# Kernel tuning notes

Measured on AMD Instinct MI355X. Metric: run time of the kernel, lower is better.

The kernel has to match this reference:

```python
import jax, jax.numpy as jnp
import numpy as np

N, N1, N2, K = 65536, 16384, 8192, 16
INDIM, HID, OUT = 64, 32, 128


def _knn_np(pos, q, k, chunk=1024):
    # brute-force chunked KNN (indices into pos) for setup only
    out = []
    for s in range(0, q.shape[0], chunk):
        d = ((q[s:s + chunk, None, :] - pos[None, :, :]) ** 2).sum(-1)
        out.append(np.argpartition(d, k, axis=1)[:, :k])
    return np.concatenate(out, 0)


def setup_inputs() -> dict:
    key = jax.random.key(0)
    ks = jax.random.split(key, 12)
    x = jax.random.normal(ks[0], (N, INDIM), jnp.float32)
    pos = jax.random.uniform(ks[1], (N, 3), jnp.float32)

    pos_np = np.asarray(pos)
    rng = np.random.default_rng(0)
    idx1 = np.sort(rng.choice(N, N1, replace=False))            # RandomSampler(ratio1)
    nn1 = _knn_np(pos_np, pos_np[idx1], K)                      # [N1, K] into full cloud
    src1, dst1 = nn1.reshape(-1), np.repeat(np.arange(N1), K)
    pos1 = pos_np[idx1]
    idx2 = np.sort(rng.choice(N1, N2, replace=False))           # RandomSampler(ratio2)
    nn2 = _knn_np(pos1, pos1[idx2], K)                          # [N2, K] into level-1 cloud
    src2, dst2 = nn2.reshape(-1), np.repeat(np.arange(N2), K)

    def lin(k, i, o):
        return jax.random.normal(k, (i, o), jnp.float32) / float(np.sqrt(i))

    return dict(
        x=x, pos=pos,
        W_down=lin(ks[2], INDIM, HID), b_down=jnp.zeros((HID,), jnp.float32),
        W_pp1=lin(ks[3], 10, 32), b_pp1=jnp.zeros((32,), jnp.float32),
        W_att1=lin(ks[4], 64, 64), b_att1=jnp.zeros((64,), jnp.float32),
        W_g1=lin(ks[5], 64, 64), b_g1=jnp.zeros((64,), jnp.float32),
        W_pp2=lin(ks[6], 10, 64), b_pp2=jnp.zeros((64,), jnp.float32),
        W_att2=lin(ks[7], 128, 128), b_att2=jnp.zeros((128,), jnp.float32),
        W_g2=lin(ks[8], 128, 128), b_g2=jnp.zeros((128,), jnp.float32),
        W_up=lin(ks[9], 128, OUT), b_up=jnp.zeros((OUT,), jnp.float32),
        W_sc=lin(ks[10], INDIM, OUT), b_sc=jnp.zeros((OUT,), jnp.float32),
        idx1=jnp.asarray(idx1, jnp.int32), idx2=jnp.asarray(idx2, jnp.int32),
        src1=jnp.asarray(src1, jnp.int32), dst1=jnp.asarray(dst1, jnp.int32),
        src2=jnp.asarray(src2, jnp.int32), dst2=jnp.asarray(dst2, jnp.int32),
    )


def _mlp(h, W, b):
    return jax.nn.relu(h @ W + b)


def _randla_conv(x, pos_all, pos_q, src, dst, Wpp, bpp, Watt, batt, Wg, bg, n_out):
    # RandlaKernel.message + add-aggregate + update (bipartite: targets = sampled points)
    pos_i, pos_j = pos_q[dst], pos_all[src]                     # [E,3]
    vij = pos_i - pos_j
    dij = jnp.sqrt((vij * vij).sum(-1, keepdims=True))          # [E,1]
    rel = jnp.concatenate([pos_i, pos_j, vij, dij], axis=1)     # [E,10]
    rij = _mlp(rel, Wpp, bpp)                                   # point_pos_nn
    fij = jnp.concatenate([x[src], rij], axis=1)                # [E, c+d]
    s = jax.nn.softmax(_mlp(fij, Watt, batt), axis=-1)          # softmax over feature dim (as in source)
    agg = jax.ops.segment_sum(s * fij, dst, num_segments=n_out) # aggr='add'
    return _mlp(agg, Wg, bg)                                    # global_nn


def reference(x, pos, W_down, b_down, W_pp1, b_pp1, W_att1, b_att1, W_g1, b_g1,
              W_pp2, b_pp2, W_att2, b_att2, W_g2, b_g2, W_up, b_up, W_sc, b_sc,
              idx1, idx2, src1, dst1, src2, dst2):
    h = _mlp(x, W_down, b_down)                                 # features_downsample (indim -> outdim//4)
    pos1 = pos[idx1]
    h = _randla_conv(h, pos, pos1, src1, dst1, W_pp1, b_pp1, W_att1, b_att1, W_g1, b_g1, N1)
    pos2 = pos1[idx2]
    h = _randla_conv(h, pos1, pos2, src2, dst2, W_pp2, b_pp2, W_att2, b_att2, W_g2, b_g2, N2)
    h = _mlp(h, W_up, b_up)                                     # features_upsample
    sc = _mlp(x[idx1][idx2], W_sc, b_sc)                        # shortcut resized, idx = idx1[idx2]
    return jax.nn.relu(h + sc)
```

## Files before the change

kernel.cpp:

```cpp
#include <hip/hip_runtime.h>

#define N_FULL 65536
#define NN1    16384
#define NN2    8192

typedef __attribute__((ext_vector_type(8))) short bf16x8;
typedef __attribute__((ext_vector_type(4))) float f32x4;
typedef unsigned short ushortT;

#define MFMA16(acc, a, b) acc = __builtin_amdgcn_mfma_f32_16x16x32_bf16(a, b, acc, 0, 0, 0)

#if __has_builtin(__builtin_amdgcn_cvt_pk_bf16_f32)
typedef __attribute__((ext_vector_type(2))) __bf16 bf16x2t;
static __device__ __forceinline__ unsigned pack2(float a, float b) {
    union { bf16x2t v; unsigned u; } c;
    c.v = __builtin_amdgcn_cvt_pk_bf16_f32(a, b);
    return c.u;
}
static __device__ __forceinline__ ushortT f2bf(float f) {
    union { bf16x2t v; ushortT s[2]; } c;
    c.v = __builtin_amdgcn_cvt_pk_bf16_f32(f, 0.f);
    return c.s[0];
}
#else
static __device__ __forceinline__ ushortT f2bf(float f) {
    union { float f; unsigned u; } v; v.f = f;
    unsigned r = v.u + 0x7FFFu + ((v.u >> 16) & 1u);
    return (ushortT)(r >> 16);
}
static __device__ __forceinline__ unsigned pack2(float a, float b) {
    return (unsigned)f2bf(a) | ((unsigned)f2bf(b) << 16);
}
#endif

static __device__ __forceinline__ float bfu2f(ushortT h) {
    union { unsigned u; float f; } v; v.u = (unsigned)h << 16; return v.f;
}

#define WS_WAT1  2304
#define WS_WGT1  6912
#define WS_WAT2  11520
#define WS_WGT2  28928
#define WS_WUPT  46336
#define WS_WSCT  63744
#define WS_H0    73728
#define WS_H1    (WS_H0 + 65536u*32u)

#define SMAX_SHIFT 24.0f

static __device__ __forceinline__ void tpose(
    const float* __restrict__ src, ushortT* __restrict__ dst,
    int K, int N, int STR, int gid, int gs)
{
    for (int i = gid; i < K * N; i += gs) {
        const int n = i / K, k = i - n * K;
        dst[n * STR + k] = f2bf(src[(size_t)k * N + n]);
    }
}

__global__ __launch_bounds__(256) void k_down(
    const float* __restrict__ x, const float* __restrict__ Wd,
    const float* __restrict__ bd,
    const float* __restrict__ Wa1, const float* __restrict__ Wg1,
    const float* __restrict__ Wa2, const float* __restrict__ Wg2,
    const float* __restrict__ Wup, const float* __restrict__ Wsc,
    ushortT* __restrict__ wsw, ushortT* __restrict__ h0w)
{
    const int t = threadIdx.x;
    if (blockIdx.x >= 512) {
        const int gid = (blockIdx.x - 512) * 256 + t, gs = 68 * 256;
        tpose(Wa1, wsw + WS_WAT1, 64, 64, 72, gid, gs);
        tpose(Wg1, wsw + WS_WGT1, 64, 64, 72, gid, gs);
        tpose(Wa2, wsw + WS_WAT2, 128, 128, 136, gid, gs);
        tpose(Wg2, wsw + WS_WGT2, 128, 128, 136, gid, gs);
        tpose(Wup, wsw + WS_WUPT, 128, 128, 136, gid, gs);
        tpose(Wsc, wsw + WS_WSCT, 64, 128, 72, gid, gs);
        return;
    }

    __shared__ __align__(16) ushortT Al[128 * 72];
    __shared__ __align__(16) ushortT Bl[32 * 72];
    const int rowBase = blockIdx.x * 128;

    {
        const int r = t >> 1, c0 = (t & 1) * 32;
        unsigned* dst = (unsigned*)Al + r * 36 + (c0 >> 1);
        const float* src = &x[(size_t)(rowBase + r) * 64 + c0];
#pragma unroll
        for (int j = 0; j < 32; j += 4) {
            const float4 v = *reinterpret_cast<const float4*>(src + j);
            dst[(j >> 1) + 0] = pack2(v.x, v.y);
            dst[(j >> 1) + 1] = pack2(v.z, v.w);
        }
        const int n = t >> 3, kc = (t & 7) * 8;
        float v[8];
#pragma unroll
        for (int j = 0; j < 8; ++j) v[j] = Wd[(size_t)(kc + j) * 32 + n];
        uint4 p;
        p.x = pack2(v[0], v[1]); p.y = pack2(v[2], v[3]);
        p.z = pack2(v[4], v[5]); p.w = pack2(v[6], v[7]);
        *(uint4*)((unsigned*)Bl + n * 36 + (kc >> 1)) = p;
    }
    __syncthreads();

    const int lane = t & 63, w = t >> 6, quad = lane >> 4, c16 = lane & 15;
    f32x4 acc[2][2];
#pragma unroll
    for (int mt = 0; mt < 2; ++mt)
#pragma unroll
        for (int nt = 0; nt < 2; ++nt)
#pragma unroll
            for (int r = 0; r < 4; ++r) acc[mt][nt][r] = 0.f;
#pragma unroll
    for (int ks = 0; ks < 2; ++ks) {
        bf16x8 a[2], b[2];
#pragma unroll
        for (int mt = 0; mt < 2; ++mt)
            a[mt] = *(const bf16x8*)&Al[(w * 32 + mt * 16 + c16) * 72 + ks * 32 + quad * 8];
#pragma unroll
        for (int nt = 0; nt < 2; ++nt)
            b[nt] = *(const bf16x8*)&Bl[(nt * 16 + c16) * 72 + ks * 32 + quad * 8];
#pragma unroll
        for (int mt = 0; mt < 2; ++mt)
#pragma unroll
            for (int nt = 0; nt < 2; ++nt) MFMA16(acc[mt][nt], a[mt], b[nt]);
    }
#pragma unroll
    for (int nt = 0; nt < 2; ++nt) {
        const int col = nt * 16 + c16;
        const float bias = bd[col];
#pragma unroll
        for (int mt = 0; mt < 2; ++mt)
#pragma unroll
            for (int r = 0; r < 4; ++r) {
                const int row = rowBase + w * 32 + mt * 16 + quad * 4 + r;
                h0w[(size_t)row * 32 + col] = f2bf(fmaxf(acc[mt][nt][r] + bias, 0.f));
            }
    }
}

__global__ __launch_bounds__(512) void k_conv1(
    const ushortT* __restrict__ h0w, const float* __restrict__ pos,
    const int* __restrict__ idx1, const int* __restrict__ src1,
    const float* __restrict__ Wpp, const float* __restrict__ bpp,
    const ushortT* __restrict__ wsw, const float* __restrict__ batt,
    const float* __restrict__ bg, ushortT* __restrict__ h1w)
{
    __shared__ __align__(16) ushortT Fl[128 * 72];
    __shared__ __align__(16) ushortT A2ls[16 * 72];
    __shared__ float Pl[352];
    const int t = threadIdx.x;
    const int d0 = blockIdx.x * 8;

    for (int i = t; i < 352; i += 512) Pl[i] = (i < 320) ? Wpp[i] : bpp[i - 320];
    for (int i = t; i < 288; i += 512) ((unsigned*)A2ls)[288 + i] = 0;

    {
        const int e = t >> 2, q = t & 3;
        const int g = e >> 4;
        const int s = src1[(d0 + g) * 16 + (e & 15)];
        ((uint4*)((unsigned*)Fl + e * 36))[q] =
            ((const uint4*)((const unsigned*)h0w + (size_t)s * 16))[q];

        const int pin = idx1[d0 + g];
        const float pix = pos[pin * 3 + 0], piy = pos[pin * 3 + 1], piz = pos[pin * 3 + 2];
        const float pjx = pos[s * 3 + 0],  pjy = pos[s * 3 + 1],  pjz = pos[s * 3 + 2];
        const float vx = pix - pjx, vy = piy - pjy, vz = piz - pjz;
        const float dij = sqrtf(vx * vx + vy * vy + vz * vz);
        const float rel[10] = {pix, piy, piz, pjx, pjy, pjz, vx, vy, vz, dij};
        __syncthreads();
        const int c0 = q * 8;
#pragma unroll
        for (int c = 0; c < 8; c += 2) {
            float a0 = Pl[320 + c0 + c], a1 = Pl[320 + c0 + c + 1];
#pragma unroll
            for (int i = 0; i < 10; ++i) {
                a0 += rel[i] * Pl[i * 32 + c0 + c];
                a1 += rel[i] * Pl[i * 32 + c0 + c + 1];
            }
            ((unsigned*)Fl)[(e * 72 + 32 + c0 + c) >> 1] = pack2(fmaxf(a0, 0.f), fmaxf(a1, 0.f));
        }
    }
    __syncthreads();

    const int lane = t & 63, w = t >> 6, quad = lane >> 4, c16 = lane & 15;
    const ushortT* WB = wsw + WS_WAT1;
    f32x4 acc[4];
#pragma unroll
    for (int nt = 0; nt < 4; ++nt)
#pragma unroll
        for (int r = 0; r < 4; ++r) acc[nt][r] = 0.f;
#pragma unroll
    for (int ks = 0; ks < 2; ++ks) {
        const bf16x8 a = *(const bf16x8*)&Fl[(w * 16 + c16) * 72 + ks * 32 + quad * 8];
#pragma unroll
        for (int nt = 0; nt < 4; ++nt) {
            const bf16x8 b = *(const bf16x8*)&WB[(nt * 16 + c16) * 72 + ks * 32 + quad * 8];
            MFMA16(acc[nt], a, b);
        }
    }
    float bcol[4];
#pragma unroll
    for (int nt = 0; nt < 4; ++nt) bcol[nt] = batt[nt * 16 + c16];

    float rs[4];
#pragma unroll
    for (int r = 0; r < 4; ++r) {
        float sm = 0.f;
#pragma unroll
        for (int nt = 0; nt < 4; ++nt) {
            const float a = fmaxf(acc[nt][r] + bcol[nt], 0.f);
            acc[nt][r] = __expf(a - SMAX_SHIFT);
            sm += acc[nt][r];
        }
        sm += __shfl_xor(sm, 1);
        sm += __shfl_xor(sm, 2);
        sm += __shfl_xor(sm, 4);
        sm += __shfl_xor(sm, 8);
        rs[r] = 1.f / sm;
    }
#pragma unroll
    for (int nt = 0; nt < 4; ++nt) {
        float v = 0.f;
#pragma unroll
        for (int r = 0; r < 4; ++r) {
            const float fv = bfu2f(Fl[(w * 16 + quad * 4 + r) * 72 + nt * 16 + c16]);
            v += acc[nt][r] * rs[r] * fv;
        }
        v += __shfl_xor(v, 16);
        v += __shfl_xor(v, 32);
        if (lane < 16)
            A2ls[w * 72 + nt * 16 + c16] = f2bf(v);
    }
    __syncthreads();

    if (w < 4) {
        const ushortT* GB = wsw + WS_WGT1;
        f32x4 acc2 = {0.f, 0.f, 0.f, 0.f};
#pragma unroll
        for (int ks = 0; ks < 2; ++ks) {
            const bf16x8 a = *(const bf16x8*)&A2ls[c16 * 72 + ks * 32 + quad * 8];
            const bf16x8 b = *(const bf16x8*)&GB[(w * 16 + c16) * 72 + ks * 32 + quad * 8];
            MFMA16(acc2, a, b);
        }
        const int col = w * 16 + c16;
        const float bias = bg[col];
        if (quad < 2) {
#pragma unroll
            for (int r = 0; r < 4; ++r) {
                const int row = quad * 4 + r;
                h1w[(size_t)(d0 + row) * 64 + col] = f2bf(fmaxf(acc2[r] + bias, 0.f));
            }
        }
    }
}

__global__ __launch_bounds__(512) void k_conv2f(
    const ushortT* __restrict__ h1w, const float* __restrict__ pos,
    const float* __restrict__ x,
    const int* __restrict__ idx1, const int* __restrict__ idx2,
    const int* __restrict__ src2,
    const float* __restrict__ Wpp, const float* __restrict__ bpp,
    const ushortT* __restrict__ wsw, const float* __restrict__ batt,
    const float* __restrict__ bg, const float* __restrict__ bup,
    const float* __restrict__ bsc, float* __restrict__ out)
{
    __shared__ __align__(16) ushortT Fl[128 * 136];
    __shared__ __align__(16) ushortT AGG[16 * 136];
    __shared__ __align__(16) ushortT H2[16 * 136];
    __shared__ float Pl[704];
    const int t = threadIdx.x;
    const int d0 = blockIdx.x * 8;

    for (int i = t; i < 704; i += 512) Pl[i] = (i < 640) ? Wpp[i] : bpp[i - 640];
    for (int i = t; i < 544; i += 512) ((unsigned*)AGG)[544 + i] = 0;

    {
        const int e = t >> 2, q = t & 3;
        const int g = e >> 4;
        const int s = src2[(d0 + g) * 16 + (e & 15)];
        {
            const uint4* srcp = (const uint4*)((const unsigned*)h1w + (size_t)s * 32);
            uint4* dstp = (uint4*)((unsigned*)Fl + e * 68);
            dstp[q * 2 + 0] = srcp[q * 2 + 0];
            dstp[q * 2 + 1] = srcp[q * 2 + 1];
        }
        const int pin = idx1[idx2[d0 + g]];
        const int sn = idx1[s];
        const float pix = pos[pin * 3 + 0], piy = pos[pin * 3 + 1], piz = pos[pin * 3 + 2];
        const float pjx = pos[sn * 3 + 0],  pjy = pos[sn * 3 + 1],  pjz = pos[sn * 3 + 2];
        const float vx = pix - pjx, vy = piy - pjy, vz = piz - pjz;
        const float dij = sqrtf(vx * vx + vy * vy + vz * vz);
        const float rel[10] = {pix, piy, piz, pjx, pjy, pjz, vx, vy, vz, dij};
        __syncthreads();
        const int c0 = q * 16;
#pragma unroll
        for (int c = 0; c < 16; c += 2) {
            float a0 = Pl[640 + c0 + c], a1 = Pl[640 + c0 + c + 1];
#pragma unroll
            for (int i = 0; i < 10; ++i) {
                a0 += rel[i] * Pl[i * 64 + c0 + c];
                a1 += rel[i] * Pl[i * 64 + c0 + c + 1];
            }
            ((unsigned*)Fl)[(e * 136 + 64 + c0 + c) >> 1] = pack2(fmaxf(a0, 0.f), fmaxf(a1, 0.f));
        }
    }
    __syncthreads();

    const int lane = t & 63, w = t >> 6, quad = lane >> 4, c16 = lane & 15;
    const ushortT* WB = wsw + WS_WAT2;
    f32x4 acc[8];
#pragma unroll
    for (int nt = 0; nt < 8; ++nt)
#pragma unroll
        for (int r = 0; r < 4; ++r) acc[nt][r] = 0.f;
#pragma unroll
    for (int ks = 0; ks < 4; ++ks) {
        const bf16x8 a = *(const bf16x8*)&Fl[(w * 16 + c16) * 136 + ks * 32 + quad * 8];
#pragma unroll
        for (int nt = 0; nt < 8; ++nt) {
            const bf16x8 b = *(const bf16x8*)&WB[(nt * 16 + c16) * 136 + ks * 32 + quad * 8];
            MFMA16(acc[nt], a, b);
        }
    }
    float bcol[8];
#pragma unroll
    for (int nt = 0; nt < 8; ++nt) bcol[nt] = batt[nt * 16 + c16];

    float rs[4];
#pragma unroll
    for (int r = 0; r < 4; ++r) {
        float sm = 0.f;
#pragma unroll
        for (int nt = 0; nt < 8; ++nt) {
            const float a = fmaxf(acc[nt][r] + bcol[nt], 0.f);
            acc[nt][r] = __expf(a - SMAX_SHIFT);
            sm += acc[nt][r];
        }
        sm += __shfl_xor(sm, 1);
        sm += __shfl_xor(sm, 2);
        sm += __shfl_xor(sm, 4);
        sm += __shfl_xor(sm, 8);
        rs[r] = 1.f / sm;
    }
#pragma unroll
    for (int nt = 0; nt < 8; ++nt) {
        float v = 0.f;
#pragma unroll
        for (int r = 0; r < 4; ++r) {
            const float fv = bfu2f(Fl[(w * 16 + quad * 4 + r) * 136 + nt * 16 + c16]);
            v += acc[nt][r] * rs[r] * fv;
        }
        v += __shfl_xor(v, 16);
        v += __shfl_xor(v, 32);
        if (lane < 16)
            AGG[w * 136 + nt * 16 + c16] = f2bf(v);
    }
    __syncthreads();


    {
        const ushortT* GB = wsw + WS_WGT2;
        f32x4 g = {0.f, 0.f, 0.f, 0.f};
#pragma unroll
        for (int ks = 0; ks < 4; ++ks) {
            const bf16x8 a = *(const bf16x8*)&AGG[c16 * 136 + ks * 32 + quad * 8];
            const bf16x8 b = *(const bf16x8*)&GB[(w * 16 + c16) * 136 + ks * 32 + quad * 8];
            MFMA16(g, a, b);
        }
        const int col = w * 16 + c16;
        const float bias = bg[col];
#pragma unroll
        for (int r = 0; r < 4; ++r)
            H2[(quad * 4 + r) * 136 + col] = f2bf(fmaxf(g[r] + bias, 0.f));
    }
    __syncthreads();

    f32x4 u = {0.f, 0.f, 0.f, 0.f};
    {
        const ushortT* UB = wsw + WS_WUPT;
#pragma unroll
        for (int ks = 0; ks < 4; ++ks) {
            const bf16x8 a = *(const bf16x8*)&H2[c16 * 136 + ks * 32 + quad * 8];
            const bf16x8 b = *(const bf16x8*)&UB[(w * 16 + c16) * 136 + ks * 32 + quad * 8];
            MFMA16(u, a, b);
        }
        const float bias = bup[w * 16 + c16];
#pragma unroll
        for (int r = 0; r < 4; ++r) u[r] = fmaxf(u[r] + bias, 0.f);
    }

    {
        const ushortT* SB = wsw + WS_WSCT;
        const int pinx = idx1[idx2[d0 + (c16 & 7)]];
        const float* xrow = &x[(size_t)pinx * 64];
        f32x4 s = {0.f, 0.f, 0.f, 0.f};
#pragma unroll
        for (int ks = 0; ks < 2; ++ks) {
            const float4 v0 = *reinterpret_cast<const float4*>(xrow + ks * 32 + quad * 8);
            const float4 v1 = *reinterpret_cast<const float4*>(xrow + ks * 32 + quad * 8 + 4);
            union { bf16x8 v; unsigned u[4]; } a;
            a.u[0] = pack2(v0.x, v0.y); a.u[1] = pack2(v0.z, v0.w);
            a.u[2] = pack2(v1.x, v1.y); a.u[3] = pack2(v1.z, v1.w);
            const bf16x8 b = *(const bf16x8*)&SB[(w * 16 + c16) * 72 + ks * 32 + quad * 8];
            MFMA16(s, a.v, b);
        }
        if (quad < 2) {
            const int col = w * 16 + c16;
            const float bias = bsc[col];
#pragma unroll
            for (int r = 0; r < 4; ++r) {
                const float sc = fmaxf(s[r] + bias, 0.f);
                out[(size_t)(d0 + quad * 4 + r) * 128 + col] = u[r] + sc;
            }
        }
    }
}

extern "C" void kernel_launch(void* const* d_in, const int* in_sizes, int n_in,
                              void* d_out, int out_size, void* d_ws, size_t ws_size,
                              hipStream_t stream)
{
    const float* x      = (const float*)d_in[0];
    const float* pos    = (const float*)d_in[1];
    const float* W_down = (const float*)d_in[2];
    const float* b_down = (const float*)d_in[3];
    const float* W_pp1  = (const float*)d_in[4];
    const float* b_pp1  = (const float*)d_in[5];
    const float* W_att1 = (const float*)d_in[6];
    const float* b_att1 = (const float*)d_in[7];
    const float* W_g1   = (const float*)d_in[8];
    const float* b_g1   = (const float*)d_in[9];
    const float* W_pp2  = (const float*)d_in[10];
    const float* b_pp2  = (const float*)d_in[11];
    const float* W_att2 = (const float*)d_in[12];
    const float* b_att2 = (const float*)d_in[13];
    const float* W_g2   = (const float*)d_in[14];
    const float* b_g2   = (const float*)d_in[15];
    const float* W_up   = (const float*)d_in[16];
    const float* b_up   = (const float*)d_in[17];
    const float* W_sc   = (const float*)d_in[18];
    const float* b_sc   = (const float*)d_in[19];
    const int* idx1 = (const int*)d_in[20];
    const int* idx2 = (const int*)d_in[21];
    const int* src1 = (const int*)d_in[22];
    const int* src2 = (const int*)d_in[24];

    ushortT* wsw = (ushortT*)d_ws;
    ushortT* h0w = wsw + WS_H0;
    ushortT* h1w = wsw + WS_H1;

    k_down  <<<512 + 68, 256, 0, stream>>>(x, W_down, b_down,
                                           W_att1, W_g1, W_att2, W_g2, W_up, W_sc,
                                           wsw, h0w);
    k_conv1 <<<NN1 / 8, 512, 0, stream>>>(h0w, pos, idx1, src1,
                                          W_pp1, b_pp1, wsw, b_att1, b_g1, h1w);
    k_conv2f<<<NN2 / 8, 512, 0, stream>>>(h1w, pos, x, idx1, idx2, src2,
                                          W_pp2, b_pp2, wsw, b_att2,
                                          b_g2, b_up, b_sc, (float*)d_out);
}
```

Before: 170.9 us.

## Fuse downsample MLP into conv1 by recomputing it per gathered neighbor

Removes the standalone downsample GEMM kernel and its bf16 h0 intermediate buffer. Each conv1 wave now gathers the neighbor rows of fp32 x directly and runs the 64->32 down projection with MFMA before the attention stage. Weight transposes, now including W_down, move into a small prep kernel. This saves one full write and read of the intermediate and one stage boundary. In exchange the down projection is recomputed for every edge (about four times the points) and each gathered row is a larger fp32 read.

Measured after the change: 173.3 us. Within noise of the previous version (+1.4%).

```diff
diff --git a/kernel.cpp b/kernel.cpp
--- a/kernel.cpp
+++ b/kernel.cpp
@@ -37,14 +37,14 @@
     union { unsigned u; float f; } v; v.u = (unsigned)h << 16; return v.f;
 }
 
+#define WS_WDT   0
 #define WS_WAT1  2304
 #define WS_WGT1  6912
 #define WS_WAT2  11520
 #define WS_WGT2  28928
 #define WS_WUPT  46336
 #define WS_WSCT  63744
-#define WS_H0    73728
-#define WS_H1    (WS_H0 + 65536u*32u)
+#define WS_H1    73728
 
 #define SMAX_SHIFT 24.0f
 
@@ -58,90 +58,26 @@
     }
 }
 
-__global__ __launch_bounds__(256) void k_down(
-    const float* __restrict__ x, const float* __restrict__ Wd,
+__global__ __launch_bounds__(256) void k_prep(
+    const float* __restrict__ Wd,  const float* __restrict__ Wa1,
+    const float* __restrict__ Wg1, const float* __restrict__ Wa2,
+    const float* __restrict__ Wg2, const float* __restrict__ Wup,
+    const float* __restrict__ Wsc, ushortT* __restrict__ wsw)
+{
+    const int gid = blockIdx.x * 256 + threadIdx.x, gs = gridDim.x * 256;
+    tpose(Wd,  wsw + WS_WDT,  64, 32, 72, gid, gs);
+    tpose(Wa1, wsw + WS_WAT1, 64, 64, 72, gid, gs);
+    tpose(Wg1, wsw + WS_WGT1, 64, 64, 72, gid, gs);
+    tpose(Wa2, wsw + WS_WAT2, 128, 128, 136, gid, gs);
+    tpose(Wg2, wsw + WS_WGT2, 128, 128, 136, gid, gs);
+    tpose(Wup, wsw + WS_WUPT, 128, 128, 136, gid, gs);
+    tpose(Wsc, wsw + WS_WSCT, 64, 128, 72, gid, gs);
+}
+
+__global__ __launch_bounds__(512) void k_conv1(
+    const float* __restrict__ x, const float* __restrict__ pos,
+    const int* __restrict__ idx1, const int* __restrict__ src1,
     const float* __restrict__ bd,
-    const float* __restrict__ Wa1, const float* __restrict__ Wg1,
-    const float* __restrict__ Wa2, const float* __restrict__ Wg2,
-    const float* __restrict__ Wup, const float* __restrict__ Wsc,
-    ushortT* __restrict__ wsw, ushortT* __restrict__ h0w)
-{
-    const int t = threadIdx.x;
-    if (blockIdx.x >= 512) {
-        const int gid = (blockIdx.x - 512) * 256 + t, gs = 68 * 256;
-        tpose(Wa1, wsw + WS_WAT1, 64, 64, 72, gid, gs);
-        tpose(Wg1, wsw + WS_WGT1, 64, 64, 72, gid, gs);
-        tpose(Wa2, wsw + WS_WAT2, 128, 128, 136, gid, gs);
-        tpose(Wg2, wsw + WS_WGT2, 128, 128, 136, gid, gs);
-        tpose(Wup, wsw + WS_WUPT, 128, 128, 136, gid, gs);
-        tpose(Wsc, wsw + WS_WSCT, 64, 128, 72, gid, gs);
-        return;
-    }
-
-    __shared__ __align__(16) ushortT Al[128 * 72];
-    __shared__ __align__(16) ushortT Bl[32 * 72];
-    const int rowBase = blockIdx.x * 128;
-
-    {
-        const int r = t >> 1, c0 = (t & 1) * 32;
-        unsigned* dst = (unsigned*)Al + r * 36 + (c0 >> 1);
-        const float* src = &x[(size_t)(rowBase + r) * 64 + c0];
-#pragma unroll
-        for (int j = 0; j < 32; j += 4) {
-            const float4 v = *reinterpret_cast<const float4*>(src + j);
-            dst[(j >> 1) + 0] = pack2(v.x, v.y);
-            dst[(j >> 1) + 1] = pack2(v.z, v.w);
-        }
-        const int n = t >> 3, kc = (t & 7) * 8;
-        float v[8];
-#pragma unroll
-        for (int j = 0; j < 8; ++j) v[j] = Wd[(size_t)(kc + j) * 32 + n];
-        uint4 p;
-        p.x = pack2(v[0], v[1]); p.y = pack2(v[2], v[3]);
-        p.z = pack2(v[4], v[5]); p.w = pack2(v[6], v[7]);
-        *(uint4*)((unsigned*)Bl + n * 36 + (kc >> 1)) = p;
-    }
-    __syncthreads();
-
-    const int lane = t & 63, w = t >> 6, quad = lane >> 4, c16 = lane & 15;
-    f32x4 acc[2][2];
-#pragma unroll
-    for (int mt = 0; mt < 2; ++mt)
-#pragma unroll
-        for (int nt = 0; nt < 2; ++nt)
-#pragma unroll
-            for (int r = 0; r < 4; ++r) acc[mt][nt][r] = 0.f;
-#pragma unroll
-    for (int ks = 0; ks < 2; ++ks) {
-        bf16x8 a[2], b[2];
-#pragma unroll
-        for (int mt = 0; mt < 2; ++mt)
-            a[mt] = *(const bf16x8*)&Al[(w * 32 + mt * 16 + c16) * 72 + ks * 32 + quad * 8];
-#pragma unroll
-        for (int nt = 0; nt < 2; ++nt)
-            b[nt] = *(const bf16x8*)&Bl[(nt * 16 + c16) * 72 + ks * 32 + quad * 8];
-#pragma unroll
-        for (int mt = 0; mt < 2; ++mt)
-#pragma unroll
-            for (int nt = 0; nt < 2; ++nt) MFMA16(acc[mt][nt], a[mt], b[nt]);
-    }
-#pragma unroll
-    for (int nt = 0; nt < 2; ++nt) {
-        const int col = nt * 16 + c16;
-        const float bias = bd[col];
-#pragma unroll
-        for (int mt = 0; mt < 2; ++mt)
-#pragma unroll
-            for (int r = 0; r < 4; ++r) {
-                const int row = rowBase + w * 32 + mt * 16 + quad * 4 + r;
-                h0w[(size_t)row * 32 + col] = f2bf(fmaxf(acc[mt][nt][r] + bias, 0.f));
-            }
-    }
-}
-
-__global__ __launch_bounds__(512) void k_conv1(
-    const ushortT* __restrict__ h0w, const float* __restrict__ pos,
-    const int* __restrict__ idx1, const int* __restrict__ src1,
     const float* __restrict__ Wpp, const float* __restrict__ bpp,
     const ushortT* __restrict__ wsw, const float* __restrict__ batt,
     const float* __restrict__ bg, ushortT* __restrict__ h1w)
@@ -151,6 +87,7 @@
     __shared__ float Pl[352];
     const int t = threadIdx.x;
     const int d0 = blockIdx.x * 8;
+    const int lane = t & 63, w = t >> 6, quad = lane >> 4, c16 = lane & 15;
 
     for (int i = t; i < 352; i += 512) Pl[i] = (i < 320) ? Wpp[i] : bpp[i - 320];
     for (int i = t; i < 288; i += 512) ((unsigned*)A2ls)[288 + i] = 0;
@@ -159,9 +96,6 @@
         const int e = t >> 2, q = t & 3;
         const int g = e >> 4;
         const int s = src1[(d0 + g) * 16 + (e & 15)];
-        ((uint4*)((unsigned*)Fl + e * 36))[q] =
-            ((const uint4*)((const unsigned*)h0w + (size_t)s * 16))[q];
-
         const int pin = idx1[d0 + g];
         const float pix = pos[pin * 3 + 0], piy = pos[pin * 3 + 1], piz = pos[pin * 3 + 2];
         const float pjx = pos[s * 3 + 0],  pjy = pos[s * 3 + 1],  pjz = pos[s * 3 + 2];
@@ -181,9 +115,40 @@
             ((unsigned*)Fl)[(e * 72 + 32 + c0 + c) >> 1] = pack2(fmaxf(a0, 0.f), fmaxf(a1, 0.f));
         }
     }
+
+    {
+        const int s = src1[(d0 + w) * 16 + c16];
+        const float* xrow = &x[(size_t)s * 64];
+        const ushortT* DB = wsw + WS_WDT;
+        f32x4 dn[2];
+#pragma unroll
+        for (int nt = 0; nt < 2; ++nt)
+#pragma unroll
+            for (int r = 0; r < 4; ++r) dn[nt][r] = 0.f;
+#pragma unroll
+        for (int ks = 0; ks < 2; ++ks) {
+            const float4 v0 = *reinterpret_cast<const float4*>(xrow + ks * 32 + quad * 8);
+            const float4 v1 = *reinterpret_cast<const float4*>(xrow + ks * 32 + quad * 8 + 4);
+            union { bf16x8 v; unsigned u[4]; } a;
+            a.u[0] = pack2(v0.x, v0.y); a.u[1] = pack2(v0.z, v0.w);
+            a.u[2] = pack2(v1.x, v1.y); a.u[3] = pack2(v1.z, v1.w);
+#pragma unroll
+            for (int nt = 0; nt < 2; ++nt) {
+                const bf16x8 b = *(const bf16x8*)&DB[(nt * 16 + c16) * 72 + ks * 32 + quad * 8];
+                MFMA16(dn[nt], a.v, b);
+            }
+        }
+#pragma unroll
+        for (int nt = 0; nt < 2; ++nt) {
+            const int col = nt * 16 + c16;
+            const float bias = bd[col];
+#pragma unroll
+            for (int r = 0; r < 4; ++r)
+                Fl[(w * 16 + quad * 4 + r) * 72 + col] = f2bf(fmaxf(dn[nt][r] + bias, 0.f));
+        }
+    }
     __syncthreads();
 
-    const int lane = t & 63, w = t >> 6, quad = lane >> 4, c16 = lane & 15;
     const ushortT* WB = wsw + WS_WAT1;
     f32x4 acc[4];
 #pragma unroll
@@ -447,13 +412,10 @@
     const int* src2 = (const int*)d_in[24];
 
     ushortT* wsw = (ushortT*)d_ws;
-    ushortT* h0w = wsw + WS_H0;
     ushortT* h1w = wsw + WS_H1;
 
-    k_down  <<<512 + 68, 256, 0, stream>>>(x, W_down, b_down,
-                                           W_att1, W_g1, W_att2, W_g2, W_up, W_sc,
-                                           wsw, h0w);
-    k_conv1 <<<NN1 / 8, 512, 0, stream>>>(h0w, pos, idx1, src1,
+    k_prep  <<<68, 256, 0, stream>>>(W_down, W_att1, W_g1, W_att2, W_g2, W_up, W_sc, wsw);
+    k_conv1 <<<NN1 / 8, 512, 0, stream>>>(x, pos, idx1, src1, b_down,
                                           W_pp1, b_pp1, wsw, b_att1, b_g1, h1w);
     k_conv2f<<<NN2 / 8, 512, 0, stream>>>(h1w, pos, x, idx1, idx2, src2,
                                           W_pp2, b_pp2, wsw, b_att2,
```
